# Performance work log

Hardware: AMD Instinct MI355X
Metric: run time of the kernel (lower is better)

The kernel has to match this reference:

```python
import jax, jax.numpy as jnp
import numpy as np

D_MODEL = 2048
NUM_Q_HEADS = 32
NUM_KV_HEADS = 8
HEAD_DIM = D_MODEL // NUM_Q_HEADS  # 64
NUM_GROUPS = NUM_Q_HEADS // NUM_KV_HEADS  # 4


def setup_inputs() -> dict:
    key = jax.random.key(0)
    ks = jax.random.split(key, 9)
    s = 1.0 / np.sqrt(D_MODEL)
    x = jax.random.normal(ks[0], (2, 2048, D_MODEL), dtype=jnp.float32)
    Wq = jax.random.uniform(ks[1], (D_MODEL, NUM_Q_HEADS * HEAD_DIM), jnp.float32, -s, s)
    bq = jax.random.uniform(ks[2], (NUM_Q_HEADS * HEAD_DIM,), jnp.float32, -s, s)
    Wk = jax.random.uniform(ks[3], (D_MODEL, NUM_KV_HEADS * HEAD_DIM), jnp.float32, -s, s)
    bk = jax.random.uniform(ks[4], (NUM_KV_HEADS * HEAD_DIM,), jnp.float32, -s, s)
    Wv = jax.random.uniform(ks[5], (D_MODEL, NUM_KV_HEADS * HEAD_DIM), jnp.float32, -s, s)
    bv = jax.random.uniform(ks[6], (NUM_KV_HEADS * HEAD_DIM,), jnp.float32, -s, s)
    Wo = jax.random.uniform(ks[7], (D_MODEL, D_MODEL), jnp.float32, -s, s)
    bo = jax.random.uniform(ks[8], (D_MODEL,), jnp.float32, -s, s)
    return {"x": x, "Wq": Wq, "bq": bq, "Wk": Wk, "bk": bk,
            "Wv": Wv, "bv": bv, "Wo": Wo, "bo": bo}


def reference(x, Wq, bq, Wk, bk, Wv, bv, Wo, bo):
    B, T, C = x.shape
    Hkv, G, Dh = NUM_KV_HEADS, NUM_GROUPS, HEAD_DIM
    # projections
    q = (x @ Wq + bq).reshape(B, T, Hkv, G, Dh)   # group G query heads per kv head
    k = (x @ Wk + bk).reshape(B, T, Hkv, Dh)
    v = (x @ Wv + bv).reshape(B, T, Hkv, Dh)
    scale = 1.0 / np.sqrt(Dh).astype(np.float32)
    # scores: [B, Hkv, G, T, T] (kv head broadcast over its G query heads)
    scores = jnp.einsum('btkgd,bskd->bkgts', q, k) * scale
    attn = jax.nn.softmax(scores, axis=-1)
    out = jnp.einsum('bkgts,bskd->btkgd', attn, v).reshape(B, T, C)
    return out @ Wo + bo
```

## Files before the change

kernel.cpp:

```cpp
#include <hip/hip_runtime.h>
#include <cstdint>
#include <cstddef>
#include <math.h>

typedef uint16_t bf16;
typedef __attribute__((ext_vector_type(8))) __bf16 bf16x8;
typedef __attribute__((ext_vector_type(2))) float f32x2;
typedef __attribute__((ext_vector_type(4))) float f32x4;
typedef __attribute__((ext_vector_type(16))) float f32x16;

#define MFMA16(a,b,c) __builtin_amdgcn_mfma_f32_16x16x32_bf16((a),(b),(c),0,0,0)
#define MFMA32(a,b,c) __builtin_amdgcn_mfma_f32_32x32x16_bf16((a),(b),(c),0,0,0)

__device__ __forceinline__ uint16_t f2bf(float f){
  uint32_t u = __float_as_uint(f);
  return (uint16_t)((u + 0x7fffu + ((u >> 16) & 1u)) >> 16);
}
__device__ __forceinline__ uint32_t pk2(float lo, float hi){
  return (uint32_t)f2bf(lo) | ((uint32_t)f2bf(hi) << 16);
}

__device__ __forceinline__ void gload_lds16(const void* g, void* l){
  __builtin_amdgcn_global_load_lds((const __attribute__((address_space(1))) void*)g,
                                   (__attribute__((address_space(3))) void*)l, 16, 0, 0);
}

__global__ void k_convert(const float* __restrict__ in, bf16* __restrict__ out, int n){
  int i = (blockIdx.x * 256 + threadIdx.x) * 4;
  if (i >= n) return;
  float4 v = *reinterpret_cast<const float4*>(in + i);
  uint32_t lo = pk2(v.x, v.y);
  uint32_t hi = pk2(v.z, v.w);
  uint2 pkv = make_uint2(lo, hi);
  *reinterpret_cast<uint2*>(out + i) = pkv;
}

__global__ void k_transposeW(const float* __restrict__ in, bf16* __restrict__ out, int R, int C){
  __shared__ float tile[64][65];
  int c0 = blockIdx.x * 64, r0 = blockIdx.y * 64;
  int t = threadIdx.x;
  int fx = t & 15, fy = t >> 4;
  #pragma unroll
  for (int i = 0; i < 4; i++){
    int r = fy + i*16;
    float4 v = *reinterpret_cast<const float4*>(in + (size_t)(r0 + r)*C + c0 + fx*4);
    tile[r][fx*4+0] = v.x; tile[r][fx*4+1] = v.y;
    tile[r][fx*4+2] = v.z; tile[r][fx*4+3] = v.w;
  }
  __syncthreads();
  int gx = t & 7, gy = t >> 3;
  #pragma unroll
  for (int i = 0; i < 2; i++){
    int c = gy + i*32;
    int rr = gx*8;
    union { bf16 h[8]; uint4 u; } pk_;
    #pragma unroll
    for (int j = 0; j < 8; j++) pk_.h[j] = f2bf(tile[rr+j][c]);
    *reinterpret_cast<uint4*>(out + (size_t)(c0 + c)*R + r0 + rr) = pk_.u;
  }
}

__device__ __forceinline__ void gemm256_core(
    const bf16* __restrict__ Abase, const bf16* __restrict__ Btbase,
    char* lds, f32x4 acc[8][4])
{
  const int tid = threadIdx.x;
  const int wid = tid >> 6, lane = tid & 63;
  const int wm = wid >> 2, wn = wid & 3;
  const int lr = lane & 15, lg = lane >> 4;
  const f32x4 vzero = {0.f, 0.f, 0.f, 0.f};
  #pragma unroll
  for (int m = 0; m < 8; m++)
    #pragma unroll
    for (int n = 0; n < 4; n++)
      acc[m][n] = vzero;

  int srcH[2];
  #pragma unroll
  for (int i = 0; i < 2; i++){
    int db = i*8192 + tid*16;
    int row = db >> 7, sp = (db >> 4) & 7, sl = sp ^ (row & 7);
    srcH[i] = row*2048 + sl*8;
  }
  const int dOf = wid*1024;

  int ksl[2];
  #pragma unroll
  for (int ks = 0; ks < 2; ks++) ksl[ks] = (((ks*4 + lg) ^ (lr & 7)) << 4);
  const int aB = wm*16384 + lr*128;
  const int bB = 32768 + (wn >> 1)*16384 + (wn & 1)*8192 + lr*128;

  const bf16* Ab1 = Abase + 128*2048;
  const bf16* Bb1 = Btbase + 128*2048;

  #define STG_HALF(dstOff, gsrc) do { \
    gload_lds16((gsrc) + srcH[0], lds + (dstOff) + dOf); \
    gload_lds16((gsrc) + srcH[1], lds + (dstOff) + 8192 + dOf); \
  } while(0)

  STG_HALF(0,     Abase);
  STG_HALF(16384, Ab1);
  STG_HALF(32768, Btbase);
  STG_HALF(49152, Bb1);
  STG_HALF(65536, Abase + 64);
  asm volatile("s_waitcnt vmcnt(2)" ::: "memory");
  __builtin_amdgcn_s_barrier();

  bf16x8 afr[4][2], bfr[4][2];
  for (int t = 0; t < 32; t++){
    const int bo = (t & 1) * 65536;
    const int nb = bo ^ 65536;

    #pragma unroll
    for (int am = 0; am < 4; am++)
      #pragma unroll
      for (int ks = 0; ks < 2; ks++)
        afr[am][ks] = *reinterpret_cast<const bf16x8*>(lds + bo + aB + am*2048 + ksl[ks]);
    #pragma unroll
    for (int bn = 0; bn < 2; bn++)
      #pragma unroll
      for (int ks = 0; ks < 2; ks++)
        bfr[bn][ks] = *reinterpret_cast<const bf16x8*>(lds + bo + bB + bn*2048 + ksl[ks]);
    if (t < 31) STG_HALF(nb + 16384, Ab1 + (t+1)*64);
    __builtin_amdgcn_s_barrier();
    asm volatile("s_waitcnt lgkmcnt(0)" ::: "memory");
    __builtin_amdgcn_sched_barrier(0);
    __builtin_amdgcn_s_setprio(1);
    #pragma unroll
    for (int am = 0; am < 4; am++)
      #pragma unroll
      for (int bn = 0; bn < 2; bn++)
        #pragma unroll
        for (int ks = 0; ks < 2; ks++)
          acc[am][bn] = MFMA16(afr[am][ks], bfr[bn][ks], acc[am][bn]);
    __builtin_amdgcn_s_setprio(0);
    __builtin_amdgcn_s_barrier();

    #pragma unroll
    for (int bn = 2; bn < 4; bn++)
      #pragma unroll
      for (int ks = 0; ks < 2; ks++)
        bfr[bn][ks] = *reinterpret_cast<const bf16x8*>(lds + bo + bB + bn*2048 + ksl[ks]);
    if (t < 31) STG_HALF(nb + 32768, Btbase + (t+1)*64);
    __builtin_amdgcn_s_barrier();
    asm volatile("s_waitcnt lgkmcnt(0)" ::: "memory");
    __builtin_amdgcn_sched_barrier(0);
    __builtin_amdgcn_s_setprio(1);
    #pragma unroll
    for (int am = 0; am < 4; am++)
      #pragma unroll
      for (int bn = 2; bn < 4; bn++)
        #pragma unroll
        for (int ks = 0; ks < 2; ks++)
          acc[am][bn] = MFMA16(afr[am][ks], bfr[bn][ks], acc[am][bn]);
    __builtin_amdgcn_s_setprio(0);
    __builtin_amdgcn_s_barrier();

    #pragma unroll
    for (int am = 0; am < 4; am++)
      #pragma unroll
      for (int ks = 0; ks < 2; ks++)
        afr[am][ks] = *reinterpret_cast<const bf16x8*>(lds + bo + aB + (am+4)*2048 + ksl[ks]);
    if (t < 31) STG_HALF(nb + 49152, Bb1 + (t+1)*64);
    __builtin_amdgcn_s_barrier();
    asm volatile("s_waitcnt lgkmcnt(0)" ::: "memory");
    __builtin_amdgcn_sched_barrier(0);
    __builtin_amdgcn_s_setprio(1);
    #pragma unroll
    for (int am = 0; am < 4; am++)
      #pragma unroll
      for (int bn = 0; bn < 2; bn++)
        #pragma unroll
        for (int ks = 0; ks < 2; ks++)
          acc[am+4][bn] = MFMA16(afr[am][ks], bfr[bn][ks], acc[am+4][bn]);
    __builtin_amdgcn_s_setprio(0);
    __builtin_amdgcn_s_barrier();

    if (t < 30) STG_HALF(bo, Abase + (t+2)*64);
    __builtin_amdgcn_s_barrier();
    __builtin_amdgcn_s_setprio(1);
    #pragma unroll
    for (int am = 0; am < 4; am++)
      #pragma unroll
      for (int bn = 2; bn < 4; bn++)
        #pragma unroll
        for (int ks = 0; ks < 2; ks++)
          acc[am+4][bn] = MFMA16(afr[am][ks], bfr[bn][ks], acc[am+4][bn]);
    __builtin_amdgcn_s_setprio(0);
    if (t < 30)      asm volatile("s_waitcnt vmcnt(2)" ::: "memory");
    else if (t == 30) asm volatile("s_waitcnt vmcnt(0)" ::: "memory");
    __builtin_amdgcn_sched_barrier(0);
    __builtin_amdgcn_s_barrier();
  }
  #undef STG_HALF
}

__device__ __forceinline__ void gemm256x128_core(
    const bf16* __restrict__ Abase, const bf16* __restrict__ Btbase,
    char* lds, f32x4 acc[8][2])
{
  const int tid = threadIdx.x;
  const int wid = tid >> 6, lane = tid & 63;
  const int wm = wid >> 2, wn = wid & 3;
  const int lr = lane & 15, lg = lane >> 4;
  const f32x4 vzero = {0.f, 0.f, 0.f, 0.f};
  #pragma unroll
  for (int m = 0; m < 8; m++)
    #pragma unroll
    for (int n = 0; n < 2; n++)
      acc[m][n] = vzero;

  int srcA[4], srcB[2];
  #pragma unroll
  for (int i = 0; i < 4; i++){
    int db = i*8192 + tid*16;
    int row = db >> 7, sp = (db >> 4) & 7, sl = sp ^ (row & 7);
    srcA[i] = row*2048 + sl*8;
  }
  #pragma unroll
  for (int i = 0; i < 2; i++){
    int db = i*8192 + tid*16;
    int row = db >> 7, sp = (db >> 4) & 7, sl = sp ^ (row & 7);
    srcB[i] = row*2048 + sl*8;
  }
  const int dOf = wid*1024;

  int ksl[2];
  #pragma unroll
  for (int ks = 0; ks < 2; ks++) ksl[ks] = (((ks*4 + lg) ^ (lr & 7)) << 4);
  const int aB = wm*16384 + lr*128;
  const int bB = wn*4096 + lr*128;

  #define STG_A(bufOff, koff) do { \
    gload_lds16(Abase + (koff) + srcA[0], lds + (bufOff) + dOf); \
    gload_lds16(Abase + (koff) + srcA[1], lds + (bufOff) + 8192 + dOf); \
    gload_lds16(Abase + (koff) + srcA[2], lds + (bufOff) + 16384 + dOf); \
    gload_lds16(Abase + (koff) + srcA[3], lds + (bufOff) + 24576 + dOf); \
  } while(0)
  #define STG_B(bufOff, koff) do { \
    gload_lds16(Btbase + (koff) + srcB[0], lds + (bufOff) + dOf); \
    gload_lds16(Btbase + (koff) + srcB[1], lds + (bufOff) + 8192 + dOf); \
  } while(0)

  STG_A(0, 0);
  STG_B(98304, 0);
  STG_A(32768, 64);
  asm volatile("s_waitcnt vmcnt(4)" ::: "memory");
  __builtin_amdgcn_s_barrier();

  bf16x8 afr[8], bfr[2];
  int aOff = 0;
  for (int t = 0; t < 32; t++){
    const int bOff = 98304 + (t & 1)*16384;
    const int aNxt2 = (aOff == 65536) ? 0 : aOff + 32768;
    const int aStg = (aOff == 0) ? 65536 : aOff - 32768;

    #pragma unroll
    for (int am = 0; am < 8; am++)
      afr[am] = *reinterpret_cast<const bf16x8*>(lds + aOff + aB + am*2048 + ksl[0]);
    #pragma unroll
    for (int bn = 0; bn < 2; bn++)
      bfr[bn] = *reinterpret_cast<const bf16x8*>(lds + bOff + bB + bn*2048 + ksl[0]);
    if (t < 31) STG_B(bOff ^ 16384, (t+1)*64);
    __builtin_amdgcn_s_barrier();
    asm volatile("s_waitcnt lgkmcnt(0)" ::: "memory");
    __builtin_amdgcn_sched_barrier(0);
    __builtin_amdgcn_s_setprio(1);
    #pragma unroll
    for (int am = 0; am < 8; am++)
      #pragma unroll
      for (int bn = 0; bn < 2; bn++)
        acc[am][bn] = MFMA16(afr[am], bfr[bn], acc[am][bn]);
    __builtin_amdgcn_s_setprio(0);
    __builtin_amdgcn_s_barrier();

    #pragma unroll
    for (int am = 0; am < 8; am++)
      afr[am] = *reinterpret_cast<const bf16x8*>(lds + aOff + aB + am*2048 + ksl[1]);
    #pragma unroll
    for (int bn = 0; bn < 2; bn++)
      bfr[bn] = *reinterpret_cast<const bf16x8*>(lds + bOff + bB + bn*2048 + ksl[1]);
    if (t < 30) STG_A(aStg, (t+2)*64);
    __builtin_amdgcn_s_barrier();
    asm volatile("s_waitcnt lgkmcnt(0)" ::: "memory");
    __builtin_amdgcn_sched_barrier(0);
    __builtin_amdgcn_s_setprio(1);
    #pragma unroll
    for (int am = 0; am < 8; am++)
      #pragma unroll
      for (int bn = 0; bn < 2; bn++)
        acc[am][bn] = MFMA16(afr[am], bfr[bn], acc[am][bn]);
    __builtin_amdgcn_s_setprio(0);
    if (t < 30)       asm volatile("s_waitcnt vmcnt(4)" ::: "memory");
    else if (t == 30) asm volatile("s_waitcnt vmcnt(0)" ::: "memory");
    __builtin_amdgcn_sched_barrier(0);
    __builtin_amdgcn_s_barrier();

    aOff = (aOff == 65536) ? 0 : aOff + 32768;
    (void)aNxt2;
  }
  #undef STG_A
  #undef STG_B
}

__global__ __launch_bounds__(512, 1) void k_qkv(
    const bf16* __restrict__ xb,
    const bf16* __restrict__ WqT, const bf16* __restrict__ WkT, const bf16* __restrict__ WvT,
    const float* __restrict__ bq, const float* __restrict__ bk, const float* __restrict__ bv,
    bf16* __restrict__ qo, bf16* __restrict__ ko, bf16* __restrict__ vtp,
    const float* __restrict__ Wo, bf16* __restrict__ WoT)
{
  __shared__ __align__(16) char lds[131072];
  int by = blockIdx.y;
  if (by >= 12){
    const int tb = (by - 12)*16 + blockIdx.x;
    const int half = threadIdx.x >> 8;
    const int t256 = threadIdx.x & 255;
    float (*tile)[65] = reinterpret_cast<float(*)[65]>(lds + half*16640);
    #pragma unroll 1
    for (int p = 0; p < 8; p++){
      int tIdx = tb*16 + p*2 + half;
      int c0 = (tIdx & 31)*64, r0 = (tIdx >> 5)*64;
      int fx = t256 & 15, fy = t256 >> 4;
      #pragma unroll
      for (int i = 0; i < 4; i++){
        int r = fy + i*16;
        float4 v = *reinterpret_cast<const float4*>(Wo + (size_t)(r0 + r)*2048 + c0 + fx*4);
        tile[r][fx*4+0] = v.x; tile[r][fx*4+1] = v.y;
        tile[r][fx*4+2] = v.z; tile[r][fx*4+3] = v.w;
      }
      __syncthreads();
      int gx = t256 & 7, gy = t256 >> 3;
      #pragma unroll
      for (int i = 0; i < 2; i++){
        int c = gy + i*32;
        int rr = gx*8;
        union { bf16 h[8]; uint4 u; } pk_;
        #pragma unroll
        for (int j = 0; j < 8; j++) pk_.h[j] = f2bf(tile[rr+j][c]);
        *reinterpret_cast<uint4*>(WoT + (size_t)(c0 + c)*2048 + r0 + rr) = pk_.u;
      }
      __syncthreads();
    }
    return;
  }
  const bf16* Bt; const float* bias; int mode; int y; float scale = 1.f;
  if (by < 8){       y = by;    Bt = WqT + (size_t)y*256*2048; bias = bq + y*256; mode = 0; scale = 0.18033688011112042f; }
  else if (by < 10){ y = by-8;  Bt = WkT + (size_t)y*256*2048; bias = bk + y*256; mode = 1; }
  else {             y = by-10; Bt = WvT + (size_t)y*256*2048; bias = bv + y*256; mode = 2; }
  int m0 = blockIdx.x * 256;
  f32x4 acc[8][4];
  gemm256_core(xb + (size_t)m0*2048, Bt, lds, acc);
  const int tid = threadIdx.x, wid = tid >> 6, lane = tid & 63;
  const int wm = wid >> 2, wn = wid & 3, lr = lane & 15, lg = lane >> 4;
  if (mode == 2){
    #pragma unroll
    for (int bn = 0; bn < 4; bn++){
      int c = wn*64 + bn*16 + lr;
      float bb = bias[c];
      int CL = y*256 + c;
      #pragma unroll
      for (int am = 0; am < 8; am++){
        int row0 = m0 + wm*128 + am*16 + lg*4;
        int bi = row0 >> 11, tl = row0 & 2047;
        union { bf16 h[4]; uint2 u; } pk_;
        #pragma unroll
        for (int r = 0; r < 4; r++) pk_.h[r] = f2bf(acc[am][bn][r] + bb);
        *reinterpret_cast<uint2*>(vtp + ((size_t)bi*512 + CL)*2048 + tl) = pk_.u;
      }
    }
  } else {
    bf16* outp = (mode == 0) ? (qo + y*256) : (ko + y*256);
    int ldc = (mode == 0) ? 2048 : 512;
    #pragma unroll
    for (int bn = 0; bn < 4; bn++){
      int c = wn*64 + bn*16 + lr;
      float bb = bias[c];
      #pragma unroll
      for (int am = 0; am < 8; am++)
        #pragma unroll
        for (int r = 0; r < 4; r++){
          int row = m0 + wm*128 + am*16 + lg*4 + r;
          outp[(size_t)row*ldc + c] = f2bf((acc[am][bn][r] + bb) * scale);
        }
    }
  }
}

__global__ __launch_bounds__(512, 1) void k_oproj(
    const bf16* __restrict__ ab, const bf16* __restrict__ WoT,
    const float* __restrict__ bo, float* __restrict__ outp)
{
  __shared__ __align__(16) char lds[131072];
  int m0 = blockIdx.x * 256, n0 = blockIdx.y * 128;
  f32x4 acc[8][2];
  gemm256x128_core(ab + (size_t)m0*2048, WoT + (size_t)n0*2048, lds, acc);
  const int tid = threadIdx.x, wid = tid >> 6, lane = tid & 63;
  const int wm = wid >> 2, wn = wid & 3, lr = lane & 15, lg = lane >> 4;
  #pragma unroll
  for (int bn = 0; bn < 2; bn++){
    int col = n0 + wn*32 + bn*16 + lr;
    float bb = bo[col];
    #pragma unroll
    for (int am = 0; am < 8; am++)
      #pragma unroll
      for (int r = 0; r < 4; r++){
        int row = m0 + wm*128 + am*16 + lg*4 + r;
        outp[(size_t)row*2048 + col] = acc[am][bn][r] + bb;
      }
  }
}

__global__ __launch_bounds__(512, 2) void k_flash(
    const bf16* __restrict__ q, const bf16* __restrict__ kmat,
    const bf16* __restrict__ vt, bf16* __restrict__ ao)
{
  __shared__ __align__(16) char lds[98304];
  const int tid = threadIdx.x;
  const int wid = tid >> 6, lane = tid & 63;
  const int l31 = lane & 31, hi = lane >> 5;
  const int bh = blockIdx.y;
  const int b = bh >> 5, hq = bh & 31, kvh = hq >> 2;
  const int qt = blockIdx.x;
  const int qrow0 = b*2048 + qt*512 + wid*64;

  bf16x8 qf[2][4];
  #pragma unroll
  for (int g = 0; g < 2; g++){
    const bf16* qrow = q + (size_t)(qrow0 + g*32 + l31)*2048 + hq*64 + hi*8;
    #pragma unroll
    for (int t = 0; t < 4; t++)
      qf[g][t] = *reinterpret_cast<const bf16x8*>(qrow + t*16);
  }

  f32x16 oacc[2][2];
  #pragma unroll
  for (int g = 0; g < 2; g++)
    #pragma unroll
    for (int n = 0; n < 2; n++)
      #pragma unroll
      for (int r = 0; r < 16; r++) oacc[g][n][r] = 0.f;
  float rsg[2][2];
  rsg[0][0]=0.f; rsg[0][1]=0.f; rsg[1][0]=0.f; rsg[1][1]=0.f;
  const f32x16 zv = {0.f,0.f,0.f,0.f,0.f,0.f,0.f,0.f,0.f,0.f,0.f,0.f,0.f,0.f,0.f,0.f};

  const int r7 = l31 & 7;
  int A[4];
  #pragma unroll
  for (int j = 0; j < 4; j++)
    A[j] = l31*128 + (((2*j + hi) ^ r7) << 4);

  const bf16* kbase = kmat + (size_t)b*2048*512 + kvh*64;
  const bf16* vbase = vt + ((size_t)b*512 + kvh*64)*2048;

  int kSrc[2], vSrc[2];
  const int dOf = wid*1024;
  #pragma unroll
  for (int i = 0; i < 2; i++){
    int kdb = i*8192 + tid*16;
    int krow = kdb >> 7, ksp = (kdb >> 4) & 7, ksl = ksp ^ (krow & 7);
    kSrc[i] = krow*512 + ksl*8;
    int o = tid*16;
    int vrow = o >> 7, vsp = (o >> 4) & 7, vsl = vsp ^ (vrow & 7);
    vSrc[i] = vrow*2048 + i*64 + vsl*8;
  }

  #define STAGE(bo, st_) do { \
    const bf16* kb_ = kbase + (size_t)(st_)*128*512; \
    const bf16* vb_ = vbase + (st_)*128; \
    gload_lds16(kb_ + kSrc[0], lds + (bo) + dOf); \
    gload_lds16(kb_ + kSrc[1], lds + (bo) + 8192 + dOf); \
    gload_lds16(vb_ + vSrc[0], lds + 49152 + (bo) + dOf); \
    gload_lds16(vb_ + vSrc[1], lds + 49152 + (bo) + 8192 + dOf); \
  } while(0)

  #define LDK(j, imm) (*reinterpret_cast<const bf16x8*>(lds + kOff + A[j] + (imm)))
  #define LDV(j, imm) (*reinterpret_cast<const bf16x8*>(lds + 49152 + kOff + A[j] + (imm)))

  STAGE(0, 0);
  STAGE(16384, 1);

  int kOff = 0;
  int sOff = 32768;
  for (int st = 0; st < 16; st++){
    if (st == 15) asm volatile("s_waitcnt vmcnt(0)" ::: "memory");
    else          asm volatile("s_waitcnt vmcnt(4)" ::: "memory");
    __builtin_amdgcn_sched_barrier(0);
    __builtin_amdgcn_s_barrier();
    __builtin_amdgcn_sched_barrier(0);
    if (st < 14){
      STAGE(sOff, st+2);
      sOff = (sOff == 32768) ? 0 : sOff + 16384;
    }

    #pragma unroll
    for (int c = 0; c < 2; c++){
      f32x16 sc[2][2];
      __builtin_amdgcn_s_setprio(1);
      #pragma unroll
      for (int t = 0; t < 4; t++){
        bf16x8 af0 = LDK(t, c*8192);
        bf16x8 af1 = LDK(t, c*8192 + 4096);
        if (t == 0){
          sc[0][0] = MFMA32(af0, qf[0][0], zv);
          sc[1][0] = MFMA32(af0, qf[1][0], zv);
          sc[0][1] = MFMA32(af1, qf[0][0], zv);
          sc[1][1] = MFMA32(af1, qf[1][0], zv);
        } else {
          sc[0][0] = MFMA32(af0, qf[0][t], sc[0][0]);
          sc[1][0] = MFMA32(af0, qf[1][t], sc[1][0]);
          sc[0][1] = MFMA32(af1, qf[0][t], sc[0][1]);
          sc[1][1] = MFMA32(af1, qf[1][t], sc[1][1]);
        }
      }
      __builtin_amdgcn_s_setprio(0);

      uint32_t pw[2][2][8];
      #pragma unroll
      for (int g = 0; g < 2; g++){
        #pragma unroll
        for (int n = 0; n < 2; n++)
          #pragma unroll
          for (int j = 0; j < 8; j++){
            float plo = __builtin_amdgcn_exp2f(sc[g][n][2*j]);
            float phi = __builtin_amdgcn_exp2f(sc[g][n][2*j+1]);
            rsg[g][j & 1] += plo + phi;
            asm("v_cvt_pk_bf16_f32 %0, %1, %2" : "=v"(pw[g][n][j]) : "v"(plo), "v"(phi));
          }
        #pragma unroll
        for (int n = 0; n < 2; n++)
          #pragma unroll
          for (int h = 0; h < 2; h++){
            asm volatile("v_permlane32_swap_b32 %0, %1" : "+v"(pw[g][n][h*4+0]), "+v"(pw[g][n][h*4+2]));
            asm volatile("v_permlane32_swap_b32 %0, %1" : "+v"(pw[g][n][h*4+1]), "+v"(pw[g][n][h*4+3]));
          }
      }

      __builtin_amdgcn_s_setprio(1);
      #pragma unroll
      for (int kk = 0; kk < 4; kk++){
        int n = kk >> 1, h = kk & 1;
        union { uint32_t w[4]; bf16x8 v; } pa0, pa1;
        #pragma unroll
        for (int w_ = 0; w_ < 4; w_++){ pa0.w[w_] = pw[0][n][h*4+w_]; pa1.w[w_] = pw[1][n][h*4+w_]; }
        #pragma unroll
        for (int nd = 0; nd < 2; nd++){
          bf16x8 vf = LDV(kk, c*8192 + nd*4096);
          oacc[0][nd] = MFMA32(pa0.v, vf, oacc[0][nd]);
          oacc[1][nd] = MFMA32(pa1.v, vf, oacc[1][nd]);
        }
      }
      __builtin_amdgcn_s_setprio(0);
    }
    kOff = (kOff == 32768) ? 0 : kOff + 16384;
  }
  #undef STAGE
  #undef LDK
  #undef LDV

  #pragma unroll
  for (int g = 0; g < 2; g++){
    float rs = rsg[g][0] + rsg[g][1];
    float l = rs + __shfl_xor(rs, 32);
    float linv = 1.f / l;
    float lv[16];
    #pragma unroll
    for (int r = 0; r < 16; r++){
      int qi = (r & 3) + 8*(r >> 2) + 4*hi;
      lv[r] = __shfl(linv, qi);
    }
    #pragma unroll
    for (int nd = 0; nd < 2; nd++)
      #pragma unroll
      for (int r = 0; r < 16; r++){
        int qi = (r & 3) + 8*(r >> 2) + 4*hi;
        int row = qrow0 + g*32 + qi;
        ao[(size_t)row*2048 + hq*64 + nd*32 + l31] = f2bf(oacc[g][nd][r] * lv[r]);
      }
  }
}

extern "C" void kernel_launch(void* const* d_in, const int* in_sizes, int n_in,
                              void* d_out, int out_size, void* d_ws, size_t ws_size,
                              hipStream_t stream)
{
  const float* x  = (const float*)d_in[0];
  const float* Wq = (const float*)d_in[1];
  const float* bq = (const float*)d_in[2];
  const float* Wk = (const float*)d_in[3];
  const float* bk = (const float*)d_in[4];
  const float* Wv = (const float*)d_in[5];
  const float* bv = (const float*)d_in[6];
  const float* Wo = (const float*)d_in[7];
  const float* bo = (const float*)d_in[8];
  float* out = (float*)d_out;

  char* ws = (char*)d_ws;
  size_t off = 0;
  auto alloc = [&](size_t bytes){ char* p = ws + off; off += (bytes + 255) & ~(size_t)255; return p; };
  bf16* xb  = (bf16*)alloc(2*2048*2048*2);
  bf16* WqT = (bf16*)alloc(2048*2048*2);
  bf16* WkT = (bf16*)alloc(512*2048*2);
  bf16* WvT = (bf16*)alloc(512*2048*2);
  bf16* WoT = (bf16*)alloc(2048*2048*2);
  bf16* qb  = (bf16*)alloc(4096*2048*2);
  bf16* kb  = (bf16*)alloc((size_t)4096*512*2);
  bf16* vtb = (bf16*)alloc((size_t)4096*512*2);
  bf16* aob = xb;

  k_convert<<<8192, 256, 0, stream>>>(x, xb, 2*2048*2048);
  k_transposeW<<<dim3(32,32), 256, 0, stream>>>(Wq, WqT, 2048, 2048);
  k_transposeW<<<dim3(8,32),  256, 0, stream>>>(Wk, WkT, 2048, 512);
  k_transposeW<<<dim3(8,32),  256, 0, stream>>>(Wv, WvT, 2048, 512);
  k_qkv<<<dim3(16,16), 512, 0, stream>>>(xb, WqT, WkT, WvT, bq, bk, bv, qb, kb, vtb, Wo, WoT);
  k_flash<<<dim3(4,64), 512, 0, stream>>>(qb, kb, vtb, aob);
  k_oproj<<<dim3(16,16), 512, 0, stream>>>(aob, WoT, bo, out);
}
```

Measured before the change: 190.0 us.

## Merge prep kernels, front-load GEMM stage loads, triple-buffer B in o-proj

Replaces the four conversion/transpose launches with one k_prep kernel that dispatches by block index, cutting launch overhead and tail gaps between small kernels. In the 256x256 GEMM core, all three half-tile global-to-LDS loads for the next k-step are issued together at the first phase, so they have more time to land. In the 256x128 o-proj core, the B operand gets a third LDS buffer and is prefetched two steps ahead, with wait counts adjusted to match. This raises LDS use to 144 KB, and the wider prefetch window may strain the memory queues or the wait-count bookkeeping.

```diff
diff --git a/kernel.cpp b/kernel.cpp
--- a/kernel.cpp
+++ b/kernel.cpp
@@ -5,7 +5,6 @@
 
 typedef uint16_t bf16;
 typedef __attribute__((ext_vector_type(8))) __bf16 bf16x8;
-typedef __attribute__((ext_vector_type(2))) float f32x2;
 typedef __attribute__((ext_vector_type(4))) float f32x4;
 typedef __attribute__((ext_vector_type(16))) float f32x16;
 
@@ -25,19 +24,9 @@
                                    (__attribute__((address_space(3))) void*)l, 16, 0, 0);
 }
 
-__global__ void k_convert(const float* __restrict__ in, bf16* __restrict__ out, int n){
-  int i = (blockIdx.x * 256 + threadIdx.x) * 4;
-  if (i >= n) return;
-  float4 v = *reinterpret_cast<const float4*>(in + i);
-  uint32_t lo = pk2(v.x, v.y);
-  uint32_t hi = pk2(v.z, v.w);
-  uint2 pkv = make_uint2(lo, hi);
-  *reinterpret_cast<uint2*>(out + i) = pkv;
-}
-
-__global__ void k_transposeW(const float* __restrict__ in, bf16* __restrict__ out, int R, int C){
-  __shared__ float tile[64][65];
-  int c0 = blockIdx.x * 64, r0 = blockIdx.y * 64;
+__device__ __forceinline__ void transpose64(const float* __restrict__ in, bf16* __restrict__ out,
+                                            int R, int C, int c0, int r0, float* tileRaw){
+  float (*tile)[65] = reinterpret_cast<float(*)[65]>(tileRaw);
   int t = threadIdx.x;
   int fx = t & 15, fy = t >> 4;
   #pragma unroll
@@ -57,6 +46,29 @@
     #pragma unroll
     for (int j = 0; j < 8; j++) pk_.h[j] = f2bf(tile[rr+j][c]);
     *reinterpret_cast<uint4*>(out + (size_t)(c0 + c)*R + r0 + rr) = pk_.u;
+  }
+}
+
+__global__ void k_prep(const float* __restrict__ x, bf16* __restrict__ xb,
+                       const float* __restrict__ Wq, bf16* __restrict__ WqT,
+                       const float* __restrict__ Wk, bf16* __restrict__ WkT,
+                       const float* __restrict__ Wv, bf16* __restrict__ WvT){
+  __shared__ __align__(16) float tile[64*65];
+  int b = blockIdx.x;
+  if (b < 8192){
+    int i = (b * 256 + threadIdx.x) * 4;
+    float4 v = *reinterpret_cast<const float4*>(x + i);
+    uint2 pkv = make_uint2(pk2(v.x, v.y), pk2(v.z, v.w));
+    *reinterpret_cast<uint2*>(xb + i) = pkv;
+  } else if (b < 9216){
+    int idx = b - 8192;
+    transpose64(Wq, WqT, 2048, 2048, (idx & 31)*64, (idx >> 5)*64, tile);
+  } else if (b < 9472){
+    int idx = b - 9216;
+    transpose64(Wk, WkT, 2048, 512, (idx & 7)*64, (idx >> 3)*64, tile);
+  } else {
+    int idx = b - 9472;
+    transpose64(Wv, WvT, 2048, 512, (idx & 7)*64, (idx >> 3)*64, tile);
   }
 }
 
@@ -121,7 +133,11 @@
       #pragma unroll
       for (int ks = 0; ks < 2; ks++)
         bfr[bn][ks] = *reinterpret_cast<const bf16x8*>(lds + bo + bB + bn*2048 + ksl[ks]);
-    if (t < 31) STG_HALF(nb + 16384, Ab1 + (t+1)*64);
+    if (t < 31){
+      STG_HALF(nb + 16384, Ab1 + (t+1)*64);
+      STG_HALF(nb + 32768, Btbase + (t+1)*64);
+      STG_HALF(nb + 49152, Bb1 + (t+1)*64);
+    }
     __builtin_amdgcn_s_barrier();
     asm volatile("s_waitcnt lgkmcnt(0)" ::: "memory");
     __builtin_amdgcn_sched_barrier(0);
@@ -141,7 +157,6 @@
       #pragma unroll
       for (int ks = 0; ks < 2; ks++)
         bfr[bn][ks] = *reinterpret_cast<const bf16x8*>(lds + bo + bB + bn*2048 + ksl[ks]);
-    if (t < 31) STG_HALF(nb + 32768, Btbase + (t+1)*64);
     __builtin_amdgcn_s_barrier();
     asm volatile("s_waitcnt lgkmcnt(0)" ::: "memory");
     __builtin_amdgcn_sched_barrier(0);
@@ -161,7 +176,6 @@
       #pragma unroll
       for (int ks = 0; ks < 2; ks++)
         afr[am][ks] = *reinterpret_cast<const bf16x8*>(lds + bo + aB + (am+4)*2048 + ksl[ks]);
-    if (t < 31) STG_HALF(nb + 49152, Bb1 + (t+1)*64);
     __builtin_amdgcn_s_barrier();
     asm volatile("s_waitcnt lgkmcnt(0)" ::: "memory");
     __builtin_amdgcn_sched_barrier(0);
@@ -187,7 +201,7 @@
         for (int ks = 0; ks < 2; ks++)
           acc[am+4][bn] = MFMA16(afr[am][ks], bfr[bn][ks], acc[am+4][bn]);
     __builtin_amdgcn_s_setprio(0);
-    if (t < 30)      asm volatile("s_waitcnt vmcnt(2)" ::: "memory");
+    if (t < 30)       asm volatile("s_waitcnt vmcnt(2)" ::: "memory");
     else if (t == 30) asm volatile("s_waitcnt vmcnt(0)" ::: "memory");
     __builtin_amdgcn_sched_barrier(0);
     __builtin_amdgcn_s_barrier();
@@ -242,18 +256,20 @@
     gload_lds16(Btbase + (koff) + srcB[1], lds + (bufOff) + 8192 + dOf); \
   } while(0)
 
+  STG_B(98304, 0);
   STG_A(0, 0);
-  STG_B(98304, 0);
+  STG_B(114688, 64);
   STG_A(32768, 64);
-  asm volatile("s_waitcnt vmcnt(4)" ::: "memory");
+  asm volatile("s_waitcnt vmcnt(6)" ::: "memory");
   __builtin_amdgcn_s_barrier();
 
   bf16x8 afr[8], bfr[2];
   int aOff = 0;
+  int bIdx = 0;
   for (int t = 0; t < 32; t++){
-    const int bOff = 98304 + (t & 1)*16384;
-    const int aNxt2 = (aOff == 65536) ? 0 : aOff + 32768;
+    const int bOff = 98304 + bIdx*16384;
     const int aStg = (aOff == 0) ? 65536 : aOff - 32768;
+    const int bStg = 98304 + ((bIdx == 0) ? 2 : bIdx - 1)*16384;
 
     #pragma unroll
     for (int am = 0; am < 8; am++)
@@ -261,7 +277,7 @@
     #pragma unroll
     for (int bn = 0; bn < 2; bn++)
       bfr[bn] = *reinterpret_cast<const bf16x8*>(lds + bOff + bB + bn*2048 + ksl[0]);
-    if (t < 31) STG_B(bOff ^ 16384, (t+1)*64);
+    if (t < 30) STG_B(bStg, (t+2)*64);
     __builtin_amdgcn_s_barrier();
     asm volatile("s_waitcnt lgkmcnt(0)" ::: "memory");
     __builtin_amdgcn_sched_barrier(0);
@@ -291,13 +307,13 @@
       for (int bn = 0; bn < 2; bn++)
         acc[am][bn] = MFMA16(afr[am], bfr[bn], acc[am][bn]);
     __builtin_amdgcn_s_setprio(0);
-    if (t < 30)       asm volatile("s_waitcnt vmcnt(4)" ::: "memory");
+    if (t < 30)       asm volatile("s_waitcnt vmcnt(6)" ::: "memory");
     else if (t == 30) asm volatile("s_waitcnt vmcnt(0)" ::: "memory");
     __builtin_amdgcn_sched_barrier(0);
     __builtin_amdgcn_s_barrier();
 
     aOff = (aOff == 65536) ? 0 : aOff + 32768;
-    (void)aNxt2;
+    bIdx = (bIdx == 2) ? 0 : bIdx + 1;
   }
   #undef STG_A
   #undef STG_B
@@ -391,7 +407,7 @@
     const bf16* __restrict__ ab, const bf16* __restrict__ WoT,
     const float* __restrict__ bo, float* __restrict__ outp)
 {
-  __shared__ __align__(16) char lds[131072];
+  __shared__ __align__(16) char lds[147456];
   int m0 = blockIdx.x * 256, n0 = blockIdx.y * 128;
   f32x4 acc[8][2];
   gemm256x128_core(ab + (size_t)m0*2048, WoT + (size_t)n0*2048, lds, acc);
@@ -608,10 +624,7 @@
   bf16* vtb = (bf16*)alloc((size_t)4096*512*2);
   bf16* aob = xb;
 
-  k_convert<<<8192, 256, 0, stream>>>(x, xb, 2*2048*2048);
-  k_transposeW<<<dim3(32,32), 256, 0, stream>>>(Wq, WqT, 2048, 2048);
-  k_transposeW<<<dim3(8,32),  256, 0, stream>>>(Wk, WkT, 2048, 512);
-  k_transposeW<<<dim3(8,32),  256, 0, stream>>>(Wv, WvT, 2048, 512);
+  k_prep<<<9728, 256, 0, stream>>>(x, xb, Wq, WqT, Wk, WkT, Wv, WvT);
   k_qkv<<<dim3(16,16), 512, 0, stream>>>(xb, WqT, WkT, WvT, bq, bk, bv, qb, kb, vtb, Wo, WoT);
   k_flash<<<dim3(4,64), 512, 0, stream>>>(qb, kb, vtb, aob);
   k_oproj<<<dim3(16,16), 512, 0, stream>>>(aob, WoT, bo, out);
```

New measurement: 189.6 us. About the same (-0.2%).
